# Performance work log

Hardware: AMD Instinct MI355X
Metric: run time of the kernel (lower is better)

## Reference

```python
import jax, jax.numpy as jnp
import numpy as np

START_DISP, END_DISP = 0, 192
STEP = 3
D0 = np.arange(START_DISP // 4, END_DISP // 4, STEP)  # [16] coarse disparities (1/4 res)
D1 = np.arange(-STEP + 1, STEP)                        # [5] refinement offsets


def _build_volume(feat_l, feat_r, disps):
    # Vectorized equivalent of AnyNet._build_volume_2d: for each disparity d,
    # left features at cols [0,W), right features shifted to cols [d, W+d).
    B, C, H, W = feat_l.shape
    md = int(disps.max())
    Wc = W + md
    D = len(disps)
    left = jnp.pad(feat_l, ((0, 0), (0, 0), (0, 0), (0, md)))          # [B,C,H,Wc]
    left = jnp.broadcast_to(left[:, None], (B, D, C, H, Wc))           # [B,D,C,H,Wc]
    idx = np.arange(Wc)[None, :] - disps[:, None]                      # [D,Wc] source col
    valid = jnp.asarray((idx >= 0) & (idx < W), feat_l.dtype)          # [D,Wc]
    right = feat_r[:, :, :, np.clip(idx, 0, W - 1)]                    # [B,C,H,D,Wc]
    right = jnp.transpose(right, (0, 3, 1, 2, 4)) * valid[None, :, None, None, :]
    return jnp.concatenate([left, right], axis=2)                      # [B,D,2C,H,Wc]


def _disparity_regression(x, disps):
    # disparity values, sum over channel axis (dim=2, keepdim).
    w = jax.nn.softmax(x, axis=1)
    d = jnp.asarray(disps, x.dtype).reshape(1, -1, 1, 1, 1)
    return jnp.sum(w * d, axis=2, keepdims=True)                       # [B,D,1,H,Wc]


def setup_inputs() -> dict:
    key = jax.random.key(0)
    k1, k2 = jax.random.split(key)
    B, C, H, W = 2, 64, 128, 240
    return {
        "feats_l": jax.random.normal(k1, (B, C, H, W), jnp.float32),
        "feats_r": jax.random.normal(k2, (B, C, H, W), jnp.float32),
    }


def reference(feats_l, feats_r):
    cost0 = _build_volume(feats_l, feats_r, D0)        # [2,16,128,128,285]
    disp_re_1 = _disparity_regression(cost0, D0)       # [2,16,1,128,285]
    cost1 = _build_volume(feats_l, feats_r, D1)        # [2,5,128,128,242]
    disp_re_2 = _disparity_regression(cost1, D1)       # [2,5,1,128,242]
    return disp_re_1, disp_re_2
```

## Files before the change

### kernel.cpp

```cpp
#include <hip/hip_runtime.h>

namespace {
constexpr int kB   = 2;
constexpr int kC   = 64;
constexpr int kH   = 128;
constexpr int kW   = 240;
constexpr int kD0  = 16;
constexpr int kD1  = 5;
constexpr int kWc1 = 285;
constexpr int kWc2 = 242;
constexpr int kPad = 48;
constexpr int kRow = 336;
constexpr int kRowBytes = kRow * 4;
constexpr int kCP  = 32;
constexpr int kGroups   = 3;
constexpr int kGThreads = 320;
constexpr int kThreads  = kGroups * kGThreads;
constexpr int kAcc  = kD0 + kD1;
constexpr int kRStr = kAcc * kWc1;
constexpr int kOut1 = kB * kD0 * kH * kWc1;
typedef unsigned int v2u __attribute__((ext_vector_type(2)));
typedef _Float16 h2 __attribute__((ext_vector_type(2)));

__device__ __forceinline__ unsigned int pkh(float lo, float hi) {
  return __builtin_bit_cast(unsigned int, __builtin_amdgcn_cvt_pkrtz(lo, hi));
}
__device__ __forceinline__ h2 H2(unsigned int u) {
  return __builtin_bit_cast(h2, u);
}
__device__ __forceinline__ float dot2(h2 a, h2 b, float c) {
  return __builtin_amdgcn_fdot2(a, b, c, false);
}

constexpr int rowOf(int s) { return (s % 3) * 7 + s / 3; }

__device__ __forceinline__ void procCP(
    v2u p0, v2u p1, v2u p2, v2u p3, v2u p4, v2u p5, v2u p6, v2u p7,
    v2u q0, v2u q1, float (&acc1)[kD0], float (&acc2)[kD1]) {
  const h2 t0  = H2(p0.x), t1  = H2(p0.y), t2  = H2(p1.x), t3  = H2(p1.y);
  const h2 t4  = H2(p2.x), t5  = H2(p2.y), t6  = H2(p3.x), t7  = H2(p3.y);
  const h2 t8  = H2(p4.x), t9  = H2(p4.y), t10 = H2(p5.x), t11 = H2(p5.y);
  const h2 t12 = H2(p6.x), t13 = H2(p6.y), t14 = H2(p7.x), t15 = H2(p7.y);
  const h2 u0 = H2(q0.x), u1 = H2(q0.y);
  const h2 u2 = H2(q1.x), u3 = H2(q1.y);
  const h2 s = (((t0 + t1) + (t2 + t3)) + ((t4 + t5) + (t6 + t7))) +
               (((t8 + t9) + (t10 + t11)) + ((t12 + t13) + (t14 + t15)));
  const float rlo = __builtin_amdgcn_rcpf((float)s.x);
  const float rhi = __builtin_amdgcn_rcpf((float)s.y);
  const h2 rp = H2(pkh(rlo, rhi));
  acc1[0]  = dot2(t0,  rp, acc1[0]);   acc1[1]  = dot2(t1,  rp, acc1[1]);
  acc1[2]  = dot2(t2,  rp, acc1[2]);   acc1[3]  = dot2(t3,  rp, acc1[3]);
  acc1[4]  = dot2(t4,  rp, acc1[4]);   acc1[5]  = dot2(t5,  rp, acc1[5]);
  acc1[6]  = dot2(t6,  rp, acc1[6]);   acc1[7]  = dot2(t7,  rp, acc1[7]);
  acc1[8]  = dot2(t8,  rp, acc1[8]);   acc1[9]  = dot2(t9,  rp, acc1[9]);
  acc1[10] = dot2(t10, rp, acc1[10]);  acc1[11] = dot2(t11, rp, acc1[11]);
  acc1[12] = dot2(t12, rp, acc1[12]);  acc1[13] = dot2(t13, rp, acc1[13]);
  acc1[14] = dot2(t14, rp, acc1[14]);  acc1[15] = dot2(t15, rp, acc1[15]);
  const h2 s2 = ((u0 + u1) + (u2 + u3)) + t0;
  const float r2lo = __builtin_amdgcn_rcpf((float)s2.x);
  const float r2hi = __builtin_amdgcn_rcpf((float)s2.y);
  const h2 r2p = H2(pkh(r2lo, r2hi));
  acc2[0] = dot2(u3, r2p, acc2[0]);
  acc2[1] = dot2(u2, r2p, acc2[1]);
  acc2[2] = dot2(t0, r2p, acc2[2]);
  acc2[3] = dot2(u1, r2p, acc2[3]);
  acc2[4] = dot2(u0, r2p, acc2[4]);
}

template <int CLEN>
__device__ __forceinline__ void sweepB(unsigned int addr,
                                       float (&acc1)[kD0], float (&acc2)[kD1]) {
  #pragma unroll
  for (int cc = 0; cc < CLEN; ++cc) {
    v2u p0, p1, p2, p3, p4, p5, p6, p7, q0, q1;
    asm volatile(
        "ds_read2_b32 %0, %10 offset0:45 offset1:42\n\t"
        "ds_read2_b32 %1, %10 offset0:39 offset1:36\n\t"
        "ds_read2_b32 %2, %10 offset0:33 offset1:30\n\t"
        "ds_read2_b32 %3, %10 offset0:27 offset1:24\n\t"
        "ds_read2_b32 %4, %10 offset0:21 offset1:18\n\t"
        "ds_read2_b32 %5, %10 offset0:15 offset1:12\n\t"
        "ds_read2_b32 %6, %10 offset0:9 offset1:6\n\t"
        "ds_read2_b32 %7, %10 offset0:3 offset1:0\n\t"
        "ds_read2_b32 %8, %10 offset0:43 offset1:44\n\t"
        "ds_read2_b32 %9, %10 offset0:46 offset1:47\n\t"
        "s_waitcnt lgkmcnt(0)"
        : "=&v"(p0), "=&v"(p1), "=&v"(p2), "=&v"(p3), "=&v"(p4),
          "=&v"(p5), "=&v"(p6), "=&v"(p7), "=&v"(q0), "=&v"(q1)
        : "v"(addr));
    procCP(p0, p1, p2, p3, p4, p5, p6, p7, q0, q1, acc1, acc2);
    addr += kRowBytes;
  }
}
}

__global__ __launch_bounds__(kThreads)
void anynet_disp_kernel(const float* __restrict__ fr, float* __restrict__ out) {
  __shared__ unsigned int E[kCP * kRow];
  __shared__ float P[kGroups * kRStr];
  const int bh  = blockIdx.x;
  const int b   = bh >> 7;
  const int h   = bh & 127;
  const int tid = threadIdx.x;

  const float* fr_b = fr + (size_t)b * kC * kH * kW + (size_t)h * kW;
  const int i0 = tid, i1 = tid + kThreads;
  const int cp0 = i0 / 60, xq0 = i0 % 60;
  const int cp1 = i1 / 60, xq1 = i1 % 60;
  const float4 a0 = *reinterpret_cast<const float4*>(
      fr_b + (size_t)(2 * cp0) * (kH * kW) + 4 * xq0);
  const float4 b0 = *reinterpret_cast<const float4*>(
      fr_b + (size_t)(2 * cp0 + 1) * (kH * kW) + 4 * xq0);
  const float4 a1 = *reinterpret_cast<const float4*>(
      fr_b + (size_t)(2 * cp1) * (kH * kW) + 4 * xq1);
  const float4 b1 = *reinterpret_cast<const float4*>(
      fr_b + (size_t)(2 * cp1 + 1) * (kH * kW) + 4 * xq1);
  if (tid < kCP * 24) {
    const int cp = tid / 24, q = tid % 24;
    const int j4 = (q < 12) ? q : q + 60;
    const uint4 ones = {0x3C003C00u, 0x3C003C00u, 0x3C003C00u, 0x3C003C00u};
    *reinterpret_cast<uint4*>(&E[cp * kRow + 4 * j4]) = ones;
  }
  {
    uint4 w0;
    w0.x = pkh(__expf(a0.x), __expf(b0.x));
    w0.y = pkh(__expf(a0.y), __expf(b0.y));
    w0.z = pkh(__expf(a0.z), __expf(b0.z));
    w0.w = pkh(__expf(a0.w), __expf(b0.w));
    *reinterpret_cast<uint4*>(&E[cp0 * kRow + kPad + 4 * xq0]) = w0;
    uint4 w1;
    w1.x = pkh(__expf(a1.x), __expf(b1.x));
    w1.y = pkh(__expf(a1.y), __expf(b1.y));
    w1.z = pkh(__expf(a1.z), __expf(b1.z));
    w1.w = pkh(__expf(a1.w), __expf(b1.w));
    *reinterpret_cast<uint4*>(&E[cp1 * kRow + kPad + 4 * xq1]) = w1;
  }
  __syncthreads();

  const int g = tid / kGThreads;
  const int t = tid % kGThreads;
  float acc1[kD0] = {};
  float acc2[kD1] = {};
  if (t < kWc1) {
    const unsigned int base =
        (unsigned int)(uintptr_t)(const void*)&E[t + 3];
    if (g == 0)      sweepB<11>(base, acc1, acc2);
    else if (g == 1) sweepB<11>(base + 11u * kRowBytes, acc1, acc2);
    else             sweepB<10>(base + 22u * kRowBytes, acc1, acc2);
  }
  __syncthreads();

  if (t < kWc1) {
    float* __restrict__ G = &P[g * kRStr + t];
    #pragma unroll
    for (int k = 0; k < kD0; ++k) G[rowOf(k) * kWc1] = acc1[k];
    #pragma unroll
    for (int j = 0; j < kD1; ++j) G[rowOf(kD0 + j) * kWc1] = acc2[j];
  }
  __syncthreads();

  if (t < kWc1) {
    const float* __restrict__ R0 = &P[7 * g * kWc1 + t];
    const int ob1 = (b * kD0 * kH + h) * kWc1 + t;
    #pragma unroll
    for (int i = 0; i < 5; ++i) {
      const float v = R0[i * kWc1] + R0[kRStr + i * kWc1] + R0[2 * kRStr + i * kWc1];
      const int s3 = 3 * i + g;
      out[ob1 + s3 * (kH * kWc1)] = (3.0f * (float)s3) * (4.0f + v);
    }
    {
      const float v = R0[5 * kWc1] + R0[kRStr + 5 * kWc1] + R0[2 * kRStr + 5 * kWc1];
      if (g == 0) {
        out[ob1 + 15 * (kH * kWc1)] = 45.0f * (4.0f + v);
      } else if (t < kWc2) {
        const int j = g - 1;
        out[kOut1 + ((b * kD1 + j) * kH + h) * kWc2 + t] =
            (float)(j - 2) * (64.0f / 5.0f + v);
      }
    }
    {
      const float v = R0[6 * kWc1] + R0[kRStr + 6 * kWc1] + R0[2 * kRStr + 6 * kWc1];
      if (t < kWc2) {
        const int j = g + 2;
        out[kOut1 + ((b * kD1 + j) * kH + h) * kWc2 + t] =
            (float)(j - 2) * (64.0f / 5.0f + v);
      }
    }
  }
}

extern "C" void kernel_launch(void* const* d_in, const int* in_sizes, int n_in,
                              void* d_out, int out_size, void* d_ws, size_t ws_size,
                              hipStream_t stream) {
  const float* feat_r = (const float*)d_in[1];
  float* out = (float*)d_out;
  anynet_disp_kernel<<<dim3(kB * kH), dim3(kThreads), 0, stream>>>(feat_r, out);
}
```

Baseline: 15.09 us.

## Split channel reduction across two blocks per row with atomic accumulation

Each (batch,row) is now handled by two blocks, each covering half of the channel pairs, which doubles the grid to 512 blocks and shrinks shared memory per block. Within a block, two thread groups each sweep 8 channel pairs and are combined through shared memory. The two blocks' partial sums are merged with atomicAdd into an output zeroed by a memset, and outputs known to be zero are no longer written. This is meant to fill more compute units and shorten the serial channel loop, at the cost of an extra memset launch, atomic traffic, and non-deterministic summation order.

```diff
diff --git a/kernel.cpp b/kernel.cpp
--- a/kernel.cpp
+++ b/kernel.cpp
@@ -5,6 +5,7 @@
 constexpr int kC   = 64;
 constexpr int kH   = 128;
 constexpr int kW   = 240;
+constexpr int kHW  = kH * kW;
 constexpr int kD0  = 16;
 constexpr int kD1  = 5;
 constexpr int kWc1 = 285;
@@ -12,12 +13,10 @@
 constexpr int kPad = 48;
 constexpr int kRow = 336;
 constexpr int kRowBytes = kRow * 4;
-constexpr int kCP  = 32;
-constexpr int kGroups   = 3;
-constexpr int kGThreads = 320;
-constexpr int kThreads  = kGroups * kGThreads;
-constexpr int kAcc  = kD0 + kD1;
-constexpr int kRStr = kAcc * kWc1;
+constexpr int kHCP = 16;
+constexpr int kGT  = 320;
+constexpr int kThreads = 640;
+constexpr int kCPG = 8;
 constexpr int kOut1 = kB * kD0 * kH * kWc1;
 typedef unsigned int v2u __attribute__((ext_vector_type(2)));
 typedef _Float16 h2 __attribute__((ext_vector_type(2)));
@@ -31,8 +30,6 @@
 __device__ __forceinline__ float dot2(h2 a, h2 b, float c) {
   return __builtin_amdgcn_fdot2(a, b, c, false);
 }
-
-constexpr int rowOf(int s) { return (s % 3) * 7 + s / 3; }
 
 __device__ __forceinline__ void procCP(
     v2u p0, v2u p1, v2u p2, v2u p3, v2u p4, v2u p5, v2u p6, v2u p7,
@@ -66,56 +63,35 @@
   acc2[3] = dot2(u1, r2p, acc2[3]);
   acc2[4] = dot2(u0, r2p, acc2[4]);
 }
-
-template <int CLEN>
-__device__ __forceinline__ void sweepB(unsigned int addr,
-                                       float (&acc1)[kD0], float (&acc2)[kD1]) {
-  #pragma unroll
-  for (int cc = 0; cc < CLEN; ++cc) {
-    v2u p0, p1, p2, p3, p4, p5, p6, p7, q0, q1;
-    asm volatile(
-        "ds_read2_b32 %0, %10 offset0:45 offset1:42\n\t"
-        "ds_read2_b32 %1, %10 offset0:39 offset1:36\n\t"
-        "ds_read2_b32 %2, %10 offset0:33 offset1:30\n\t"
-        "ds_read2_b32 %3, %10 offset0:27 offset1:24\n\t"
-        "ds_read2_b32 %4, %10 offset0:21 offset1:18\n\t"
-        "ds_read2_b32 %5, %10 offset0:15 offset1:12\n\t"
-        "ds_read2_b32 %6, %10 offset0:9 offset1:6\n\t"
-        "ds_read2_b32 %7, %10 offset0:3 offset1:0\n\t"
-        "ds_read2_b32 %8, %10 offset0:43 offset1:44\n\t"
-        "ds_read2_b32 %9, %10 offset0:46 offset1:47\n\t"
-        "s_waitcnt lgkmcnt(0)"
-        : "=&v"(p0), "=&v"(p1), "=&v"(p2), "=&v"(p3), "=&v"(p4),
-          "=&v"(p5), "=&v"(p6), "=&v"(p7), "=&v"(q0), "=&v"(q1)
-        : "v"(addr));
-    procCP(p0, p1, p2, p3, p4, p5, p6, p7, q0, q1, acc1, acc2);
-    addr += kRowBytes;
-  }
-}
 }
 
 __global__ __launch_bounds__(kThreads)
 void anynet_disp_kernel(const float* __restrict__ fr, float* __restrict__ out) {
-  __shared__ unsigned int E[kCP * kRow];
-  __shared__ float P[kGroups * kRStr];
-  const int bh  = blockIdx.x;
-  const int b   = bh >> 7;
-  const int h   = bh & 127;
-  const int tid = threadIdx.x;
+  __shared__ unsigned int E[kHCP * kRow];
+  __shared__ float P[(kD0 + kD1) * kGT];
+  const int blk  = blockIdx.x;
+  const int half = blk & 1;
+  const int bh   = blk >> 1;
+  const int b    = bh >> 7;
+  const int h    = bh & 127;
+  const int tid  = threadIdx.x;
 
-  const float* fr_b = fr + (size_t)b * kC * kH * kW + (size_t)h * kW;
-  const int i0 = tid, i1 = tid + kThreads;
-  const int cp0 = i0 / 60, xq0 = i0 % 60;
-  const int cp1 = i1 / 60, xq1 = i1 % 60;
+  const float* fr_b = fr + (size_t)b * kC * kHW + (size_t)h * kW;
+  const int i0 = tid;
+  const int i1 = tid + kThreads;
+  const bool v1 = (i1 < kHCP * 60);
+  const int lc0 = i0 / 60, xq0 = i0 % 60;
+  const int i1c = v1 ? i1 : (kHCP * 60 - 1);
+  const int lc1 = i1c / 60, xq1 = i1c % 60;
   const float4 a0 = *reinterpret_cast<const float4*>(
-      fr_b + (size_t)(2 * cp0) * (kH * kW) + 4 * xq0);
+      fr_b + (size_t)(2 * (kHCP * half + lc0)) * kHW + 4 * xq0);
   const float4 b0 = *reinterpret_cast<const float4*>(
-      fr_b + (size_t)(2 * cp0 + 1) * (kH * kW) + 4 * xq0);
+      fr_b + (size_t)(2 * (kHCP * half + lc0) + 1) * kHW + 4 * xq0);
   const float4 a1 = *reinterpret_cast<const float4*>(
-      fr_b + (size_t)(2 * cp1) * (kH * kW) + 4 * xq1);
+      fr_b + (size_t)(2 * (kHCP * half + lc1)) * kHW + 4 * xq1);
   const float4 b1 = *reinterpret_cast<const float4*>(
-      fr_b + (size_t)(2 * cp1 + 1) * (kH * kW) + 4 * xq1);
-  if (tid < kCP * 24) {
+      fr_b + (size_t)(2 * (kHCP * half + lc1) + 1) * kHW + 4 * xq1);
+  if (tid < kHCP * 24) {
     const int cp = tid / 24, q = tid % 24;
     const int j4 = (q < 12) ? q : q + 60;
     const uint4 ones = {0x3C003C00u, 0x3C003C00u, 0x3C003C00u, 0x3C003C00u};
@@ -127,63 +103,72 @@
     w0.y = pkh(__expf(a0.y), __expf(b0.y));
     w0.z = pkh(__expf(a0.z), __expf(b0.z));
     w0.w = pkh(__expf(a0.w), __expf(b0.w));
-    *reinterpret_cast<uint4*>(&E[cp0 * kRow + kPad + 4 * xq0]) = w0;
-    uint4 w1;
-    w1.x = pkh(__expf(a1.x), __expf(b1.x));
-    w1.y = pkh(__expf(a1.y), __expf(b1.y));
-    w1.z = pkh(__expf(a1.z), __expf(b1.z));
-    w1.w = pkh(__expf(a1.w), __expf(b1.w));
-    *reinterpret_cast<uint4*>(&E[cp1 * kRow + kPad + 4 * xq1]) = w1;
+    *reinterpret_cast<uint4*>(&E[lc0 * kRow + kPad + 4 * xq0]) = w0;
+    if (v1) {
+      uint4 w1;
+      w1.x = pkh(__expf(a1.x), __expf(b1.x));
+      w1.y = pkh(__expf(a1.y), __expf(b1.y));
+      w1.z = pkh(__expf(a1.z), __expf(b1.z));
+      w1.w = pkh(__expf(a1.w), __expf(b1.w));
+      *reinterpret_cast<uint4*>(&E[lc1 * kRow + kPad + 4 * xq1]) = w1;
+    }
   }
   __syncthreads();
 
-  const int g = tid / kGThreads;
-  const int t = tid % kGThreads;
+  const int g = tid / kGT;
+  const int t = tid % kGT;
   float acc1[kD0] = {};
   float acc2[kD1] = {};
   if (t < kWc1) {
-    const unsigned int base =
-        (unsigned int)(uintptr_t)(const void*)&E[t + 3];
-    if (g == 0)      sweepB<11>(base, acc1, acc2);
-    else if (g == 1) sweepB<11>(base + 11u * kRowBytes, acc1, acc2);
-    else             sweepB<10>(base + 22u * kRowBytes, acc1, acc2);
+    unsigned int addr = (unsigned int)(uintptr_t)(const void*)
+        &E[g * kCPG * kRow + t + 3];
+    #pragma unroll 1
+    for (int cc = 0; cc < kCPG; ++cc) {
+      v2u p0, p1, p2, p3, p4, p5, p6, p7, q0, q1;
+      asm volatile(
+          "ds_read2_b32 %0, %10 offset0:45 offset1:42\n\t"
+          "ds_read2_b32 %1, %10 offset0:39 offset1:36\n\t"
+          "ds_read2_b32 %2, %10 offset0:33 offset1:30\n\t"
+          "ds_read2_b32 %3, %10 offset0:27 offset1:24\n\t"
+          "ds_read2_b32 %4, %10 offset0:21 offset1:18\n\t"
+          "ds_read2_b32 %5, %10 offset0:15 offset1:12\n\t"
+          "ds_read2_b32 %6, %10 offset0:9 offset1:6\n\t"
+          "ds_read2_b32 %7, %10 offset0:3 offset1:0\n\t"
+          "ds_read2_b32 %8, %10 offset0:43 offset1:44\n\t"
+          "ds_read2_b32 %9, %10 offset0:46 offset1:47\n\t"
+          "s_waitcnt lgkmcnt(0)"
+          : "=&v"(p0), "=&v"(p1), "=&v"(p2), "=&v"(p3), "=&v"(p4),
+            "=&v"(p5), "=&v"(p6), "=&v"(p7), "=&v"(q0), "=&v"(q1)
+          : "v"(addr));
+      procCP(p0, p1, p2, p3, p4, p5, p6, p7, q0, q1, acc1, acc2);
+      addr += kRowBytes;
+    }
+  }
+
+  if (g == 1 && t < kWc1) {
+    #pragma unroll
+    for (int k = 0; k < kD0; ++k) P[k * kGT + t] = acc1[k];
+    #pragma unroll
+    for (int j = 0; j < kD1; ++j) P[(kD0 + j) * kGT + t] = acc2[j];
   }
   __syncthreads();
 
-  if (t < kWc1) {
-    float* __restrict__ G = &P[g * kRStr + t];
+  if (g == 0 && t < kWc1) {
+    const float cAdd = (half == 0) ? 4.0f : 0.0f;
     #pragma unroll
-    for (int k = 0; k < kD0; ++k) G[rowOf(k) * kWc1] = acc1[k];
-    #pragma unroll
-    for (int j = 0; j < kD1; ++j) G[rowOf(kD0 + j) * kWc1] = acc2[j];
-  }
-  __syncthreads();
-
-  if (t < kWc1) {
-    const float* __restrict__ R0 = &P[7 * g * kWc1 + t];
-    const int ob1 = (b * kD0 * kH + h) * kWc1 + t;
-    #pragma unroll
-    for (int i = 0; i < 5; ++i) {
-      const float v = R0[i * kWc1] + R0[kRStr + i * kWc1] + R0[2 * kRStr + i * kWc1];
-      const int s3 = 3 * i + g;
-      out[ob1 + s3 * (kH * kWc1)] = (3.0f * (float)s3) * (4.0f + v);
+    for (int d = 1; d < kD0; ++d) {
+      const float v = cAdd + acc1[d] + P[d * kGT + t];
+      atomicAdd(&out[((b * kD0 + d) * kH + h) * kWc1 + t],
+                (3.0f * (float)d) * v);
     }
-    {
-      const float v = R0[5 * kWc1] + R0[kRStr + 5 * kWc1] + R0[2 * kRStr + 5 * kWc1];
-      if (g == 0) {
-        out[ob1 + 15 * (kH * kWc1)] = 45.0f * (4.0f + v);
-      } else if (t < kWc2) {
-        const int j = g - 1;
-        out[kOut1 + ((b * kD1 + j) * kH + h) * kWc2 + t] =
-            (float)(j - 2) * (64.0f / 5.0f + v);
-      }
-    }
-    {
-      const float v = R0[6 * kWc1] + R0[kRStr + 6 * kWc1] + R0[2 * kRStr + 6 * kWc1];
-      if (t < kWc2) {
-        const int j = g + 2;
-        out[kOut1 + ((b * kD1 + j) * kH + h) * kWc2 + t] =
-            (float)(j - 2) * (64.0f / 5.0f + v);
+    if (t < kWc2) {
+      const float c2 = (half == 0) ? (64.0f / 5.0f) : 0.0f;
+      #pragma unroll
+      for (int j = 0; j < kD1; ++j) {
+        if (j == 2) continue;
+        const float v = c2 + acc2[j] + P[(kD0 + j) * kGT + t];
+        atomicAdd(&out[kOut1 + ((b * kD1 + j) * kH + h) * kWc2 + t],
+                  (float)(j - 2) * v);
       }
     }
   }
@@ -194,5 +179,6 @@
                               hipStream_t stream) {
   const float* feat_r = (const float*)d_in[1];
   float* out = (float*)d_out;
-  anynet_disp_kernel<<<dim3(kB * kH), dim3(kThreads), 0, stream>>>(feat_r, out);
+  hipMemsetAsync(out, 0, (size_t)out_size * sizeof(float), stream);
+  anynet_disp_kernel<<<dim3(kB * kH * 2), dim3(kThreads), 0, stream>>>(feat_r, out);
 }
```

Result: slower. 25.23 us (+67.1%).
